# Kernel tuning notes

Measured on AMD Instinct MI355X. Metric: run time of the kernel, lower is better.

The kernel has to match this reference:

```python
import jax, jax.numpy as jnp
import numpy as np
import math

WIN = (3, 3, 3)
DIL = 1
B, N, C = 2, 8192, 128
D = H = W = 48


def _offsets():
    # same ordering as torch get_offset_coord: row-major over (win0,win1,win2)
    half = [math.ceil(w * 0.5) - 1 for w in WIN]
    axes = [jnp.arange(-half[i], WIN[i] - half[i]) for i in range(3)]
    g = jnp.stack(jnp.meshgrid(*axes, indexing='ij'), axis=-1).reshape(-1, 3)  # (K,3)
    # dilation applies to the first two spatial dims (D,H)
    return g * jnp.array([DIL, DIL, 1], dtype=g.dtype)


def setup_inputs() -> dict:
    key = jax.random.key(0)
    ks = jax.random.split(key, 10)
    s = 1.0 / np.sqrt(C)
    return {
        'q_feat': jax.random.normal(ks[0], (B, N, C), jnp.float32),
        'feat': jax.random.normal(ks[1], (B, C, D, H, W), jnp.float32),
        'proj_coord': jax.random.randint(ks[2], (B, N, 3), 0, 48, jnp.int32),
        'hr_coord': jax.random.uniform(ks[3], (B, N, 3), jnp.float32),
        'q_w': jax.random.normal(ks[4], (C, C), jnp.float32) * s,
        'q_b': jax.random.normal(ks[5], (C,), jnp.float32) * s,
        'k_w': jax.random.normal(ks[6], (C, C), jnp.float32) * s,
        'k_b': jax.random.normal(ks[7], (C,), jnp.float32) * s,
        'v_w': jax.random.normal(ks[8], (C, C), jnp.float32) * s,
        'v_b': jax.random.normal(ks[9], (C,), jnp.float32) * s,
    }


def reference(q_feat, feat, proj_coord, hr_coord, q_w, q_b, k_w, k_b, v_w, v_b):
    b, c = feat.shape[:2]
    n = proj_coord.shape[1]
    off = _offsets()                                  # (K,3)
    K = off.shape[0]
    p = [WIN[0] // 2 * DIL, WIN[1] // 2 * DIL, WIN[2] // 2]
    # replication padding (torch ReplicationPad3d == edge mode)
    padded = jnp.pad(feat, ((0, 0), (0, 0), (p[0], p[0]), (p[1], p[1]), (p[2], p[2])), mode='edge')
    Dp, Hp, Wp = padded.shape[2:]
    # absolute window coords in padded volume: (b,N,K,3)
    coords = proj_coord[:, :, None, :] + jnp.array(p, jnp.int32) + off.astype(jnp.int32)
    flat = coords[..., 0] * (Hp * Wp) + coords[..., 1] * Wp + coords[..., 2]  # (b,N,K)
    feat_flat = padded.reshape(b, c, -1).transpose(0, 2, 1)                   # (b,S,c)
    local_feat = jnp.take_along_axis(feat_flat, flat.reshape(b, -1, 1), axis=1)
    local_feat = local_feat.reshape(b, n, K, c)
    # FBLA: q/k attention over local window
    q = q_feat @ q_w.T + q_b                          # (b,N,c)
    k = jnp.einsum('bnkc,dc->bnkd', local_feat, k_w) + k_b
    atten = jax.nn.softmax(jnp.einsum('bnd,bnkd->bnk', q, k), axis=-1)
    v = jnp.einsum('bnkc,dc->bnkd', local_feat, v_w) + v_b
    x = jnp.einsum('bnk,bnkd->bnd', atten, v)
    return q_feat + x
```

## Files before the change

### kernel.cpp

```cpp
#include <hip/hip_runtime.h>
#include <cstdint>

typedef unsigned short u16;
typedef unsigned int   u32;

__device__ __forceinline__ float bf2f(u16 u){ return __uint_as_float(((u32)u) << 16); }
__device__ __forceinline__ float bflo(u32 u){ return __uint_as_float(u << 16); }
__device__ __forceinline__ float bfhi(u32 u){ return __uint_as_float(u & 0xffff0000u); }
__device__ __forceinline__ u16 f2bf(float f){
    u32 x = __float_as_uint(f);
    u32 r = x + 0x7fffu + ((x >> 16) & 1u);
    return (u16)(r >> 16);
}
__device__ __forceinline__ int detect_bf16(const void* p){
    const u16* h = (const u16*)p;
    int hits = 0;
    for (int i = 0; i < 64; ++i){
        const int e = (h[2 * i] >> 7) & 0xFF;
        hits += (e >= 110 && e <= 140) ? 1 : 0;
    }
    return hits >= 40;
}
__device__ __forceinline__ int detect_i64(const int* p){
    int z = 0;
    for (int i = 0; i < 48; ++i) z += (p[2 * i + 1] == 0) ? 1 : 0;
    return z >= 40;
}
__device__ __forceinline__ float ldf(const void* p, size_t i, int isbf){
    return isbf ? bf2f(((const u16*)p)[i]) : ((const float*)p)[i];
}
__device__ __forceinline__ void read_proj(const int* proj, int q, int p64,
                                          int& pz, int& py, int& px){
    if (p64){
        pz = proj[(size_t)(q * 3 + 0) * 2];
        py = proj[(size_t)(q * 3 + 1) * 2];
        px = proj[(size_t)(q * 3 + 2) * 2];
    } else {
        pz = proj[q * 3 + 0]; py = proj[q * 3 + 1]; px = proj[q * 3 + 2];
    }
    pz = min(max(pz, 0), 47); py = min(max(py, 0), 47); px = min(max(px, 0), 47);
}

__global__ __launch_bounds__(256) void k_prep(const void* __restrict__ qw_,
                                              const void* __restrict__ qb_,
                                              const void* __restrict__ kw_,
                                              const void* __restrict__ vw_,
                                              float* __restrict__ M,
                                              float* __restrict__ bias,
                                              float* __restrict__ W2){
    const int bid = blockIdx.x, t = threadIdx.x;
    if (bid < 64){
        const int e = bid * 2 + (t >> 7), c = t & 127;
        const int is_qw = detect_bf16(qw_), is_kw = detect_bf16(kw_);
        float acc = 0.f;
        for (int d = 0; d < 128; ++d)
            acc += ldf(kw_, (size_t)d * 128 + c, is_kw) * ldf(qw_, (size_t)d * 128 + e, is_qw);
        M[e * 128 + c] = acc;
        if (bid == 0 && t < 128){
            const int is_qb = detect_bf16(qb_);
            float ab = 0.f;
            for (int d = 0; d < 128; ++d)
                ab += ldf(kw_, (size_t)d * 128 + t, is_kw) * ldf(qb_, d, is_qb);
            bias[t] = ab;
        }
    } else {
        const int i = (bid - 64) * 256 + t;
        const int c = i >> 7, d = i & 127;
        const int is_vw = detect_bf16(vw_);
        W2[c * 128 + d] = ldf(vw_, (size_t)d * 128 + c, is_vw);
    }
}

__global__ __launch_bounds__(256) void k_tr(const void* __restrict__ feat_,
                                            u16* __restrict__ featT){
    __shared__ u32 sh[4096];
    __shared__ int sbf;
    const int t = threadIdx.x;
    if (t == 0) sbf = detect_bf16(feat_);
    __syncthreads();
    const int isbf = sbf;
    const int chunk = blockIdx.x;
    const int b = chunk / 1728;
    const size_t rel = (size_t)(chunk - b * 1728) * 64;
    if (isbf){
        const u16* f = (const u16*)feat_;
        for (int it = 0; it < 4; ++it){
            const int i = it * 256 + t;
            const int c2 = i >> 4, q16 = i & 15;
            const size_t sA = ((size_t)(b * 128 + 2 * c2    )) * 110592 + rel + q16 * 4;
            const size_t sB = ((size_t)(b * 128 + 2 * c2 + 1)) * 110592 + rel + q16 * 4;
            const uint2 va = *reinterpret_cast<const uint2*>(f + sA);
            const uint2 vb = *reinterpret_cast<const uint2*>(f + sB);
            const u32 vals[4] = {
                (va.x & 0xffffu) | (vb.x << 16),
                (va.x >> 16)     | (vb.x & 0xffff0000u),
                (va.y & 0xffffu) | (vb.y << 16),
                (va.y >> 16)     | (vb.y & 0xffff0000u)
            };
#pragma unroll
            for (int j = 0; j < 4; ++j){
                const int v = q16 * 4 + j;
                const int xv = (v ^ (v >> 4)) & 15;
                sh[v * 64 + (c2 & 3) + 4 * ((c2 >> 2) ^ xv)] = vals[j];
            }
        }
    } else {
        const float* f = (const float*)feat_;
        for (int it = 0; it < 4; ++it){
            const int i = it * 256 + t;
            const int c2 = i >> 4, q16 = i & 15;
            const size_t sA = ((size_t)(b * 128 + 2 * c2    )) * 110592 + rel + q16 * 4;
            const size_t sB = ((size_t)(b * 128 + 2 * c2 + 1)) * 110592 + rel + q16 * 4;
            const float4 a  = *reinterpret_cast<const float4*>(f + sA);
            const float4 bv = *reinterpret_cast<const float4*>(f + sB);
            const float av[4] = {a.x, a.y, a.z, a.w};
            const float bw[4] = {bv.x, bv.y, bv.z, bv.w};
#pragma unroll
            for (int j = 0; j < 4; ++j){
                const int v = q16 * 4 + j;
                const int xv = (v ^ (v >> 4)) & 15;
                sh[v * 64 + (c2 & 3) + 4 * ((c2 >> 2) ^ xv)] =
                    (u32)f2bf(av[j]) | ((u32)f2bf(bw[j]) << 16);
            }
        }
    }
    __syncthreads();
    u32* ft = reinterpret_cast<u32*>(featT);
    const size_t obase = (size_t)chunk * 4096;
#pragma unroll
    for (int k = 0; k < 4; ++k){
        const int G = k * 256 + t;
        const int v = G >> 4, gr = G & 15;
        const int xv = (v ^ (v >> 4)) & 15;
        const uint4 val = *reinterpret_cast<const uint4*>(&sh[v * 64 + 4 * (gr ^ xv)]);
        *reinterpret_cast<uint4*>(ft + obase + (size_t)G * 4) = val;
    }
}

__global__ __launch_bounds__(256) void k_qk(const void* __restrict__ qf_,
                                            const float* __restrict__ M,
                                            const float* __restrict__ bias,
                                            float* __restrict__ qk_all){
    __shared__ float Msh[128 * 128];
    __shared__ float qT[128 * 32];
    const int t = threadIdx.x;
    const int is_qf = detect_bf16(qf_);
    const int qbase = blockIdx.x * 32;
    {
        const float4* Mg4 = reinterpret_cast<const float4*>(M);
        float4* Ms4 = reinterpret_cast<float4*>(Msh);
        for (int i = t; i < 4096; i += 256) Ms4[i] = Mg4[i];
    }
#pragma unroll
    for (int p = 0; p < 4; ++p){
        const int i = p * 256 + t;
        const int q = i & 31, gr = i >> 5;
        float v[4];
        if (is_qf){
            const ushort4 a = *reinterpret_cast<const ushort4*>((const u16*)qf_ + (size_t)(qbase + q) * 128 + gr * 4);
            v[0] = bf2f(a.x); v[1] = bf2f(a.y); v[2] = bf2f(a.z); v[3] = bf2f(a.w);
        } else {
            const float4 a = *reinterpret_cast<const float4*>((const float*)qf_ + (size_t)(qbase + q) * 128 + gr * 4);
            v[0] = a.x; v[1] = a.y; v[2] = a.z; v[3] = a.w;
        }
#pragma unroll
        for (int j = 0; j < 4; ++j) qT[(gr * 4 + j) * 32 + q] = v[j];
    }
    __syncthreads();
    const int g  = t & 31;
    const int qa = t >> 5;
    const float4 b4 = *reinterpret_cast<const float4*>(bias + g * 4);
    float4 acc0 = b4, acc1 = b4, acc2 = b4, acc3 = b4;
#pragma unroll 4
    for (int e = 0; e < 128; ++e){
        const float4 qv = *reinterpret_cast<const float4*>(&qT[e * 32 + qa * 4]);
        const float4 m  = *reinterpret_cast<const float4*>(&Msh[e * 128 + g * 4]);
        acc0.x += qv.x * m.x; acc0.y += qv.x * m.y; acc0.z += qv.x * m.z; acc0.w += qv.x * m.w;
        acc1.x += qv.y * m.x; acc1.y += qv.y * m.y; acc1.z += qv.y * m.z; acc1.w += qv.y * m.w;
        acc2.x += qv.z * m.x; acc2.y += qv.z * m.y; acc2.z += qv.z * m.z; acc2.w += qv.z * m.w;
        acc3.x += qv.w * m.x; acc3.y += qv.w * m.y; acc3.z += qv.w * m.z; acc3.w += qv.w * m.w;
    }
    float* o0 = qk_all + (size_t)(qbase + qa * 4 + 0) * 128 + g * 4;
    float* o1 = qk_all + (size_t)(qbase + qa * 4 + 1) * 128 + g * 4;
    float* o2 = qk_all + (size_t)(qbase + qa * 4 + 2) * 128 + g * 4;
    float* o3 = qk_all + (size_t)(qbase + qa * 4 + 3) * 128 + g * 4;
    *reinterpret_cast<float4*>(o0) = acc0;
    *reinterpret_cast<float4*>(o1) = acc1;
    *reinterpret_cast<float4*>(o2) = acc2;
    *reinterpret_cast<float4*>(o3) = acc3;
}

__global__ __launch_bounds__(256) void k_attn_feat(const u16* __restrict__ featT,
                                                   const float* __restrict__ qk_all,
                                                   const int* __restrict__ proj,
                                                   float* __restrict__ g){
    const int lane = threadIdx.x & 63;
    const int q = blockIdx.x * 4 + (threadIdx.x >> 6);
    const int kg = lane >> 4, cl = lane & 15;
    const int b = q >> 13;
    const int p64 = detect_i64(proj);
    int pz, py, px; read_proj(proj, q, p64, pz, py, px);
    const float4* qp4 = reinterpret_cast<const float4*>(qk_all + (size_t)q * 128 + cl * 8);
    const float4 qA = qp4[0], qB = qp4[1];
    const u16* base = featT + (size_t)b * 14155776 + cl * 8;
    uint4 fr[7];
    float sc[7];
#pragma unroll
    for (int s = 0; s < 7; ++s){
        const int k = s * 4 + kg;
        uint4 v = make_uint4(0u, 0u, 0u, 0u);
        if (k < 27){
            const int dz = k / 9, r9 = k - dz * 9, dy = r9 / 3, dx = r9 - dy * 3;
            const int zz = min(max(pz - 1 + dz, 0), 47);
            const int yy = min(max(py - 1 + dy, 0), 47);
            const int xx = min(max(px - 1 + dx, 0), 47);
            v = *reinterpret_cast<const uint4*>(base + (size_t)(zz * 2304 + yy * 48 + xx) * 128);
        }
        fr[s] = v;
        float t = qA.x * bflo(v.x) + qA.y * bfhi(v.x)
                + qA.z * bflo(v.y) + qA.w * bfhi(v.y)
                + qB.x * bflo(v.z) + qB.y * bfhi(v.z)
                + qB.z * bflo(v.w) + qB.w * bfhi(v.w);
        t += __shfl_xor(t, 1, 64);
        t += __shfl_xor(t, 2, 64);
        t += __shfl_xor(t, 4, 64);
        t += __shfl_xor(t, 8, 64);
        sc[s] = (k < 27) ? t : -1e30f;
    }
    float mx = sc[0];
#pragma unroll
    for (int s = 1; s < 7; ++s) mx = fmaxf(mx, sc[s]);
    mx = fmaxf(mx, __shfl_xor(mx, 16, 64));
    mx = fmaxf(mx, __shfl_xor(mx, 32, 64));
    float e[7], Z = 0.f;
#pragma unroll
    for (int s = 0; s < 7; ++s){ e[s] = __expf(sc[s] - mx); Z += e[s]; }
    Z += __shfl_xor(Z, 16, 64);
    Z += __shfl_xor(Z, 32, 64);
    const float inv = 1.0f / Z;
    float w[8];
#pragma unroll
    for (int i = 0; i < 8; ++i) w[i] = 0.f;
#pragma unroll
    for (int s = 0; s < 7; ++s){
        const float a = e[s] * inv;
        w[0] += a * bflo(fr[s].x); w[1] += a * bfhi(fr[s].x);
        w[2] += a * bflo(fr[s].y); w[3] += a * bfhi(fr[s].y);
        w[4] += a * bflo(fr[s].z); w[5] += a * bfhi(fr[s].z);
        w[6] += a * bflo(fr[s].w); w[7] += a * bfhi(fr[s].w);
    }
#pragma unroll
    for (int i = 0; i < 8; ++i){
        w[i] += __shfl_xor(w[i], 16, 64);
        w[i] += __shfl_xor(w[i], 32, 64);
    }
    if (kg == 0){
        float4 lo4; lo4.x = w[0]; lo4.y = w[1]; lo4.z = w[2]; lo4.w = w[3];
        float4 hi4; hi4.x = w[4]; hi4.y = w[5]; hi4.z = w[6]; hi4.w = w[7];
        float4* o = reinterpret_cast<float4*>(g + (size_t)q * 128 + cl * 8);
        o[0] = lo4; o[1] = hi4;
    }
}

__global__ __launch_bounds__(256) void k_attn_direct(const void* __restrict__ feat_,
                                                     const float* __restrict__ qk_all,
                                                     const int* __restrict__ proj,
                                                     float* __restrict__ g){
    const int lane = threadIdx.x & 63;
    const int q = blockIdx.x * 4 + (threadIdx.x >> 6);
    const int kg = lane >> 4, cl = lane & 15;
    const int b = q >> 13;
    const int isbf = detect_bf16(feat_);
    const int p64 = detect_i64(proj);
    int pz, py, px; read_proj(proj, q, p64, pz, py, px);
    const float* qk = qk_all + (size_t)q * 128 + cl * 8;
    float qv[8];
#pragma unroll
    for (int i = 0; i < 8; ++i) qv[i] = qk[i];
    const size_t cbase = ((size_t)b * 128 + cl * 8) * 110592;
    float f[7][8];
    float sc[7];
#pragma unroll
    for (int s = 0; s < 7; ++s){
        const int k = s * 4 + kg;
#pragma unroll
        for (int i = 0; i < 8; ++i) f[s][i] = 0.f;
        if (k < 27){
            const int dz = k / 9, r9 = k - dz * 9, dy = r9 / 3, dx = r9 - dy * 3;
            const int zz = min(max(pz - 1 + dz, 0), 47);
            const int yy = min(max(py - 1 + dy, 0), 47);
            const int xx = min(max(px - 1 + dx, 0), 47);
            const size_t off = (size_t)zz * 2304 + yy * 48 + xx;
#pragma unroll
            for (int i = 0; i < 8; ++i) f[s][i] = ldf(feat_, cbase + (size_t)i * 110592 + off, isbf);
        }
        float t = 0.f;
#pragma unroll
        for (int i = 0; i < 8; ++i) t += qv[i] * f[s][i];
        t += __shfl_xor(t, 1, 64);
        t += __shfl_xor(t, 2, 64);
        t += __shfl_xor(t, 4, 64);
        t += __shfl_xor(t, 8, 64);
        sc[s] = (k < 27) ? t : -1e30f;
    }
    float mx = sc[0];
#pragma unroll
    for (int s = 1; s < 7; ++s) mx = fmaxf(mx, sc[s]);
    mx = fmaxf(mx, __shfl_xor(mx, 16, 64));
    mx = fmaxf(mx, __shfl_xor(mx, 32, 64));
    float e[7], Z = 0.f;
#pragma unroll
    for (int s = 0; s < 7; ++s){ e[s] = __expf(sc[s] - mx); Z += e[s]; }
    Z += __shfl_xor(Z, 16, 64);
    Z += __shfl_xor(Z, 32, 64);
    const float inv = 1.0f / Z;
    float w[8];
#pragma unroll
    for (int i = 0; i < 8; ++i) w[i] = 0.f;
#pragma unroll
    for (int s = 0; s < 7; ++s){
        const float a = e[s] * inv;
#pragma unroll
        for (int i = 0; i < 8; ++i) w[i] += a * f[s][i];
    }
#pragma unroll
    for (int i = 0; i < 8; ++i){
        w[i] += __shfl_xor(w[i], 16, 64);
        w[i] += __shfl_xor(w[i], 32, 64);
    }
    if (kg == 0){
        float4 lo4; lo4.x = w[0]; lo4.y = w[1]; lo4.z = w[2]; lo4.w = w[3];
        float4 hi4; hi4.x = w[4]; hi4.y = w[5]; hi4.z = w[6]; hi4.w = w[7];
        float4* o = reinterpret_cast<float4*>(g + (size_t)q * 128 + cl * 8);
        o[0] = lo4; o[1] = hi4;
    }
}

__global__ __launch_bounds__(256) void k_out(const float* __restrict__ gbuf,
                                             const float* __restrict__ W2,
                                             const void* __restrict__ qf_,
                                             const void* __restrict__ vb_,
                                             float* __restrict__ out){
    __shared__ float Wsh[128 * 128];
    __shared__ float gT[128 * 32];
    const int t = threadIdx.x;
    const int is_qf = detect_bf16(qf_);
    const int is_vb = detect_bf16(vb_);
    const int qbase = blockIdx.x * 32;
    {
        const float4* Wg4 = reinterpret_cast<const float4*>(W2);
        float4* Ws4 = reinterpret_cast<float4*>(Wsh);
        for (int i = t; i < 4096; i += 256) Ws4[i] = Wg4[i];
    }
#pragma unroll
    for (int p = 0; p < 4; ++p){
        const int i = p * 256 + t;
        const int q = i & 31, gr = i >> 5;
        const float4 a = *reinterpret_cast<const float4*>(gbuf + (size_t)(qbase + q) * 128 + gr * 4);
        gT[(gr * 4 + 0) * 32 + q] = a.x;
        gT[(gr * 4 + 1) * 32 + q] = a.y;
        gT[(gr * 4 + 2) * 32 + q] = a.z;
        gT[(gr * 4 + 3) * 32 + q] = a.w;
    }
    __syncthreads();
    const int g  = t & 31;
    const int qa = t >> 5;
    float4 vb4;
    if (is_vb){
        const ushort4 v = *reinterpret_cast<const ushort4*>((const u16*)vb_ + g * 4);
        vb4.x = bf2f(v.x); vb4.y = bf2f(v.y); vb4.z = bf2f(v.z); vb4.w = bf2f(v.w);
    } else {
        vb4 = *reinterpret_cast<const float4*>((const float*)vb_ + g * 4);
    }
    float4 acc0 = vb4, acc1 = vb4, acc2 = vb4, acc3 = vb4;
#pragma unroll 4
    for (int c = 0; c < 128; ++c){
        const float4 gv = *reinterpret_cast<const float4*>(&gT[c * 32 + qa * 4]);
        const float4 m  = *reinterpret_cast<const float4*>(&Wsh[c * 128 + g * 4]);
        acc0.x += gv.x * m.x; acc0.y += gv.x * m.y; acc0.z += gv.x * m.z; acc0.w += gv.x * m.w;
        acc1.x += gv.y * m.x; acc1.y += gv.y * m.y; acc1.z += gv.y * m.z; acc1.w += gv.y * m.w;
        acc2.x += gv.z * m.x; acc2.y += gv.z * m.y; acc2.z += gv.z * m.z; acc2.w += gv.z * m.w;
        acc3.x += gv.w * m.x; acc3.y += gv.w * m.y; acc3.z += gv.w * m.z; acc3.w += gv.w * m.w;
    }
#pragma unroll
    for (int j = 0; j < 4; ++j){
        const int q = qbase + qa * 4 + j;
        float4 acc = (j == 0) ? acc0 : (j == 1) ? acc1 : (j == 2) ? acc2 : acc3;
        float4 r;
        if (is_qf){
            const ushort4 a = *reinterpret_cast<const ushort4*>((const u16*)qf_ + (size_t)q * 128 + g * 4);
            r.x = bf2f(a.x); r.y = bf2f(a.y); r.z = bf2f(a.z); r.w = bf2f(a.w);
        } else {
            r = *reinterpret_cast<const float4*>((const float*)qf_ + (size_t)q * 128 + g * 4);
        }
        acc.x += r.x; acc.y += r.y; acc.z += r.z; acc.w += r.w;
        *reinterpret_cast<float4*>(out + (size_t)q * 128 + g * 4) = acc;
    }
}

__global__ __launch_bounds__(128) void k_simple(const void* __restrict__ qf_,
                                                const void* __restrict__ feat_,
                                                const void* __restrict__ proj_,
                                                const void* __restrict__ qw_,
                                                const void* __restrict__ qb_,
                                                const void* __restrict__ kw_,
                                                const void* __restrict__ kb_,
                                                const void* __restrict__ vw_,
                                                const void* __restrict__ vb_,
                                                float* __restrict__ out){
    __shared__ float qfs[128];
    __shared__ float qs[128];
    __shared__ float ts[128];
    __shared__ float gs[128];
    __shared__ float ss4[27][4];
    __shared__ float aa[27];
    __shared__ float kbd[1];
    const int t = threadIdx.x;
    const int q = blockIdx.x;
    const int b = q >> 13;
    const int is_qf = detect_bf16(qf_);
    const int is_ft = detect_bf16(feat_);
    const int is_qw = detect_bf16(qw_);
    const int is_qb = detect_bf16(qb_);
    const int is_kw = detect_bf16(kw_);
    const int is_kb = detect_bf16(kb_);
    const int is_vw = detect_bf16(vw_);
    const int is_vb = detect_bf16(vb_);
    const int p64   = detect_i64((const int*)proj_);
    qfs[t] = ldf(qf_, (size_t)q * 128 + t, is_qf);
    __syncthreads();
    {
        float acc = ldf(qb_, t, is_qb);
        for (int e = 0; e < 128; ++e)
            acc += ldf(qw_, (size_t)t * 128 + e, is_qw) * qfs[e];
        qs[t] = acc;
    }
    __syncthreads();
    {
        float acc = 0.f;
        for (int d = 0; d < 128; ++d)
            acc += ldf(kw_, (size_t)d * 128 + t, is_kw) * qs[d];
        ts[t] = acc;
    }
    if (t == 0){
        float kd = 0.f;
        for (int d = 0; d < 128; ++d) kd += ldf(kb_, d, is_kb) * qs[d];
        kbd[0] = kd;
    }
    __syncthreads();
    int pz, py, px; read_proj((const int*)proj_, q, p64, pz, py, px);
    if (t < 108){
        const int k = t >> 2, part = t & 3;
        const int dz = k / 9, dy = (k / 3) % 3, dx = k % 3;
        const int zz = min(max(pz - 1 + dz, 0), 47);
        const int yy = min(max(py - 1 + dy, 0), 47);
        const int xx = min(max(px - 1 + dx, 0), 47);
        const size_t sp = (size_t)zz * 2304 + yy * 48 + xx;
        float s = 0.f;
        for (int c = part * 32; c < part * 32 + 32; ++c)
            s += ts[c] * ldf(feat_, ((size_t)b * 128 + c) * 110592 + sp, is_ft);
        ss4[k][part] = s;
    }
    __syncthreads();
    if (t == 0){
        float sc[27];
        float mx = -1e30f;
        for (int k = 0; k < 27; ++k){
            sc[k] = ss4[k][0] + ss4[k][1] + ss4[k][2] + ss4[k][3] + kbd[0];
            mx = fmaxf(mx, sc[k]);
        }
        float Z = 0.f;
        for (int k = 0; k < 27; ++k){ sc[k] = expf(sc[k] - mx); Z += sc[k]; }
        const float inv = 1.0f / Z;
        for (int k = 0; k < 27; ++k) aa[k] = sc[k] * inv;
    }
    __syncthreads();
    {
        float g = 0.f;
        const size_t cb = ((size_t)b * 128 + t) * 110592;
        for (int k = 0; k < 27; ++k){
            const int dz = k / 9, dy = (k / 3) % 3, dx = k % 3;
            const int zz = min(max(pz - 1 + dz, 0), 47);
            const int yy = min(max(py - 1 + dy, 0), 47);
            const int xx = min(max(px - 1 + dx, 0), 47);
            g += aa[k] * ldf(feat_, cb + (size_t)zz * 2304 + yy * 48 + xx, is_ft);
        }
        gs[t] = g;
    }
    __syncthreads();
    {
        float o = qfs[t] + ldf(vb_, t, is_vb);
        for (int c = 0; c < 128; ++c)
            o += ldf(vw_, (size_t)t * 128 + c, is_vw) * gs[c];
        out[(size_t)q * 128 + t] = o;
    }
}

extern "C" void kernel_launch(void* const* d_in, const int* in_sizes, int n_in,
                              void* d_out, int out_size, void* d_ws, size_t ws_size,
                              hipStream_t stream) {
    const void* qfeat = d_in[0];
    const void* feat  = d_in[1];
    const int*  proj  = (const int*)d_in[2];
    const void* qw = d_in[4];
    const void* qb = d_in[5];
    const void* kw = d_in[6];
    const void* kb = d_in[7];
    const void* vw = d_in[8];
    const void* vb = d_in[9];
    float* out = (float*)d_out;

    char* wsb = (char*)d_ws;
    float* M      = (float*)(wsb);
    float* bias   = (float*)(wsb + 65536);
    float* W2     = (float*)(wsb + 66048);
    float* qk_all = (float*)(wsb + 131584);
    float* g      = (float*)(wsb + 8520192);
    u16*   featT  = (u16*)  (wsb + 16908800);

    const int tier = (ws_size >= (size_t)73531904) ? 1
                   : (ws_size >= (size_t)16908800) ? 2 : 3;

    if (tier == 3){
        hipLaunchKernelGGL(k_simple, dim3(16384), dim3(128), 0, stream,
                           qfeat, feat, proj, qw, qb, kw, kb, vw, vb, out);
        return;
    }
    hipLaunchKernelGGL(k_prep, dim3(128), dim3(256), 0, stream, qw, qb, kw, vw, M, bias, W2);
    hipLaunchKernelGGL(k_qk,   dim3(512), dim3(256), 0, stream, qfeat, M, bias, qk_all);
    if (tier == 1){
        hipLaunchKernelGGL(k_tr,        dim3(3456), dim3(256), 0, stream, feat, featT);
        hipLaunchKernelGGL(k_attn_feat, dim3(4096), dim3(256), 0, stream, featT, qk_all, proj, g);
    } else {
        hipLaunchKernelGGL(k_attn_direct, dim3(4096), dim3(256), 0, stream, feat, qk_all, proj, g);
    }
    hipLaunchKernelGGL(k_out,  dim3(512), dim3(256), 0, stream, g, W2, qfeat, vb, out);
}
```

Baseline: 295.6 us.

## Use packed FP32 FMA in GEMM and attention loops, hoist dtype detection

Rewrites the inner FMA loops of the q·M GEMM, the output projection GEMM and the attention dot/weighted-sum to use v_pk_fma_f32 on float pairs, aiming to halve VALU issue count. Dtype and int64 detection, previously redone per thread in every kernel, now runs once in the prep kernel and is stored in a small flags buffer that later kernels read. The workspace offsets shift to make room for the flags. Inline asm constrains scheduling, and the feature-gather kernel is likely memory-bound, so the gain there may be limited.

```diff
diff --git a/kernel.cpp b/kernel.cpp
--- a/kernel.cpp
+++ b/kernel.cpp
@@ -3,6 +3,8 @@
 
 typedef unsigned short u16;
 typedef unsigned int   u32;
+typedef __attribute__((ext_vector_type(2))) float f32x2;
+typedef __attribute__((ext_vector_type(4))) float f32x4;
 
 __device__ __forceinline__ float bf2f(u16 u){ return __uint_as_float(((u32)u) << 16); }
 __device__ __forceinline__ float bflo(u32 u){ return __uint_as_float(u << 16); }
@@ -41,15 +43,39 @@
     pz = min(max(pz, 0), 47); py = min(max(py, 0), 47); px = min(max(px, 0), 47);
 }
 
+__device__ __forceinline__ void pk_fma_b0(f32x2& acc, const f32x2 s, const f32x2 m){
+    asm("v_pk_fma_f32 %0, %1, %2, %0 op_sel:[0,0,0] op_sel_hi:[0,1,1]"
+        : "+v"(acc) : "v"(s), "v"(m));
+}
+__device__ __forceinline__ void pk_fma_b1(f32x2& acc, const f32x2 s, const f32x2 m){
+    asm("v_pk_fma_f32 %0, %1, %2, %0 op_sel:[1,0,0] op_sel_hi:[1,1,1]"
+        : "+v"(acc) : "v"(s), "v"(m));
+}
+__device__ __forceinline__ void pk_fma(f32x2& acc, const f32x2 a, const f32x2 b){
+    asm("v_pk_fma_f32 %0, %1, %2, %0"
+        : "+v"(acc) : "v"(a), "v"(b));
+}
+
 __global__ __launch_bounds__(256) void k_prep(const void* __restrict__ qw_,
                                               const void* __restrict__ qb_,
                                               const void* __restrict__ kw_,
                                               const void* __restrict__ vw_,
+                                              const void* __restrict__ qf_,
+                                              const void* __restrict__ feat_,
+                                              const int*  __restrict__ proj_,
+                                              const void* __restrict__ vb_,
                                               float* __restrict__ M,
                                               float* __restrict__ bias,
-                                              float* __restrict__ W2){
+                                              float* __restrict__ W2,
+                                              int* __restrict__ flags){
     const int bid = blockIdx.x, t = threadIdx.x;
     if (bid < 64){
+        if (bid == 0){
+            if (t == 0)      flags[0] = detect_bf16(qf_);
+            else if (t == 1) flags[1] = detect_bf16(feat_);
+            else if (t == 2) flags[2] = detect_bf16(vb_);
+            else if (t == 3) flags[3] = detect_i64(proj_);
+        }
         const int e = bid * 2 + (t >> 7), c = t & 127;
         const int is_qw = detect_bf16(qw_), is_kw = detect_bf16(kw_);
         float acc = 0.f;
@@ -72,13 +98,11 @@
 }
 
 __global__ __launch_bounds__(256) void k_tr(const void* __restrict__ feat_,
-                                            u16* __restrict__ featT){
+                                            u16* __restrict__ featT,
+                                            const int* __restrict__ flags){
     __shared__ u32 sh[4096];
-    __shared__ int sbf;
     const int t = threadIdx.x;
-    if (t == 0) sbf = detect_bf16(feat_);
-    __syncthreads();
-    const int isbf = sbf;
+    const int isbf = flags[1];
     const int chunk = blockIdx.x;
     const int b = chunk / 1728;
     const size_t rel = (size_t)(chunk - b * 1728) * 64;
@@ -140,11 +164,12 @@
 __global__ __launch_bounds__(256) void k_qk(const void* __restrict__ qf_,
                                             const float* __restrict__ M,
                                             const float* __restrict__ bias,
-                                            float* __restrict__ qk_all){
+                                            float* __restrict__ qk_all,
+                                            const int* __restrict__ flags){
     __shared__ float Msh[128 * 128];
     __shared__ float qT[128 * 32];
     const int t = threadIdx.x;
-    const int is_qf = detect_bf16(qf_);
+    const int is_qf = flags[0];
     const int qbase = blockIdx.x * 32;
     {
         const float4* Mg4 = reinterpret_cast<const float4*>(M);
@@ -170,38 +195,45 @@
     const int g  = t & 31;
     const int qa = t >> 5;
     const float4 b4 = *reinterpret_cast<const float4*>(bias + g * 4);
-    float4 acc0 = b4, acc1 = b4, acc2 = b4, acc3 = b4;
+    const f32x2 bi01 = {b4.x, b4.y}, bi23 = {b4.z, b4.w};
+    f32x2 a00 = bi01, a01 = bi23, a10 = bi01, a11 = bi23;
+    f32x2 a20 = bi01, a21 = bi23, a30 = bi01, a31 = bi23;
 #pragma unroll 4
     for (int e = 0; e < 128; ++e){
-        const float4 qv = *reinterpret_cast<const float4*>(&qT[e * 32 + qa * 4]);
-        const float4 m  = *reinterpret_cast<const float4*>(&Msh[e * 128 + g * 4]);
-        acc0.x += qv.x * m.x; acc0.y += qv.x * m.y; acc0.z += qv.x * m.z; acc0.w += qv.x * m.w;
-        acc1.x += qv.y * m.x; acc1.y += qv.y * m.y; acc1.z += qv.y * m.z; acc1.w += qv.y * m.w;
-        acc2.x += qv.z * m.x; acc2.y += qv.z * m.y; acc2.z += qv.z * m.z; acc2.w += qv.z * m.w;
-        acc3.x += qv.w * m.x; acc3.y += qv.w * m.y; acc3.z += qv.w * m.z; acc3.w += qv.w * m.w;
-    }
-    float* o0 = qk_all + (size_t)(qbase + qa * 4 + 0) * 128 + g * 4;
-    float* o1 = qk_all + (size_t)(qbase + qa * 4 + 1) * 128 + g * 4;
-    float* o2 = qk_all + (size_t)(qbase + qa * 4 + 2) * 128 + g * 4;
-    float* o3 = qk_all + (size_t)(qbase + qa * 4 + 3) * 128 + g * 4;
-    *reinterpret_cast<float4*>(o0) = acc0;
-    *reinterpret_cast<float4*>(o1) = acc1;
-    *reinterpret_cast<float4*>(o2) = acc2;
-    *reinterpret_cast<float4*>(o3) = acc3;
+        const f32x4 qv = *reinterpret_cast<const f32x4*>(&qT[e * 32 + qa * 4]);
+        const f32x4 mv = *reinterpret_cast<const f32x4*>(&Msh[e * 128 + g * 4]);
+        const f32x2 q01 = qv.xy, q23 = qv.zw;
+        const f32x2 m01 = mv.xy, m23 = mv.zw;
+        pk_fma_b0(a00, q01, m01); pk_fma_b0(a01, q01, m23);
+        pk_fma_b1(a10, q01, m01); pk_fma_b1(a11, q01, m23);
+        pk_fma_b0(a20, q23, m01); pk_fma_b0(a21, q23, m23);
+        pk_fma_b1(a30, q23, m01); pk_fma_b1(a31, q23, m23);
+    }
+    const f32x4 r0 = {a00.x, a00.y, a01.x, a01.y};
+    const f32x4 r1 = {a10.x, a10.y, a11.x, a11.y};
+    const f32x4 r2 = {a20.x, a20.y, a21.x, a21.y};
+    const f32x4 r3 = {a30.x, a30.y, a31.x, a31.y};
+    *reinterpret_cast<f32x4*>(qk_all + (size_t)(qbase + qa * 4 + 0) * 128 + g * 4) = r0;
+    *reinterpret_cast<f32x4*>(qk_all + (size_t)(qbase + qa * 4 + 1) * 128 + g * 4) = r1;
+    *reinterpret_cast<f32x4*>(qk_all + (size_t)(qbase + qa * 4 + 2) * 128 + g * 4) = r2;
+    *reinterpret_cast<f32x4*>(qk_all + (size_t)(qbase + qa * 4 + 3) * 128 + g * 4) = r3;
 }
 
 __global__ __launch_bounds__(256) void k_attn_feat(const u16* __restrict__ featT,
                                                    const float* __restrict__ qk_all,
                                                    const int* __restrict__ proj,
-                                                   float* __restrict__ g){
+                                                   float* __restrict__ g,
+                                                   const int* __restrict__ flags){
     const int lane = threadIdx.x & 63;
     const int q = blockIdx.x * 4 + (threadIdx.x >> 6);
     const int kg = lane >> 4, cl = lane & 15;
     const int b = q >> 13;
-    const int p64 = detect_i64(proj);
+    const int p64 = flags[3];
     int pz, py, px; read_proj(proj, q, p64, pz, py, px);
     const float4* qp4 = reinterpret_cast<const float4*>(qk_all + (size_t)q * 128 + cl * 8);
     const float4 qA = qp4[0], qB = qp4[1];
+    const f32x2 qA01 = {qA.x, qA.y}, qA23 = {qA.z, qA.w};
+    const f32x2 qB01 = {qB.x, qB.y}, qB23 = {qB.z, qB.w};
     const u16* base = featT + (size_t)b * 14155776 + cl * 8;
     uint4 fr[7];
     float sc[7];
@@ -217,10 +249,14 @@
             v = *reinterpret_cast<const uint4*>(base + (size_t)(zz * 2304 + yy * 48 + xx) * 128);
         }
         fr[s] = v;
-        float t = qA.x * bflo(v.x) + qA.y * bfhi(v.x)
-                + qA.z * bflo(v.y) + qA.w * bfhi(v.y)
-                + qB.x * bflo(v.z) + qB.y * bfhi(v.z)
-                + qB.z * bflo(v.w) + qB.w * bfhi(v.w);
+        const f32x2 f0 = {bflo(v.x), bfhi(v.x)};
+        const f32x2 f1 = {bflo(v.y), bfhi(v.y)};
+        const f32x2 f2 = {bflo(v.z), bfhi(v.z)};
+        const f32x2 f3 = {bflo(v.w), bfhi(v.w)};
+        f32x2 d2 = {0.f, 0.f};
+        pk_fma(d2, qA01, f0); pk_fma(d2, qA23, f1);
+        pk_fma(d2, qB01, f2); pk_fma(d2, qB23, f3);
+        float t = d2.x + d2.y;
         t += __shfl_xor(t, 1, 64);
         t += __shfl_xor(t, 2, 64);
         t += __shfl_xor(t, 4, 64);
@@ -238,17 +274,20 @@
     Z += __shfl_xor(Z, 16, 64);
     Z += __shfl_xor(Z, 32, 64);
     const float inv = 1.0f / Z;
-    float w[8];
-#pragma unroll
-    for (int i = 0; i < 8; ++i) w[i] = 0.f;
+    f32x2 w0 = {0.f,0.f}, w1 = {0.f,0.f}, w2 = {0.f,0.f}, w3 = {0.f,0.f};
 #pragma unroll
     for (int s = 0; s < 7; ++s){
         const float a = e[s] * inv;
-        w[0] += a * bflo(fr[s].x); w[1] += a * bfhi(fr[s].x);
-        w[2] += a * bflo(fr[s].y); w[3] += a * bfhi(fr[s].y);
-        w[4] += a * bflo(fr[s].z); w[5] += a * bfhi(fr[s].z);
-        w[6] += a * bflo(fr[s].w); w[7] += a * bfhi(fr[s].w);
-    }
+        const f32x2 aa = {a, a};
+        const uint4 v = fr[s];
+        const f32x2 f0 = {bflo(v.x), bfhi(v.x)};
+        const f32x2 f1 = {bflo(v.y), bfhi(v.y)};
+        const f32x2 f2 = {bflo(v.z), bfhi(v.z)};
+        const f32x2 f3 = {bflo(v.w), bfhi(v.w)};
+        pk_fma(w0, aa, f0); pk_fma(w1, aa, f1);
+        pk_fma(w2, aa, f2); pk_fma(w3, aa, f3);
+    }
+    float w[8] = {w0.x, w0.y, w1.x, w1.y, w2.x, w2.y, w3.x, w3.y};
 #pragma unroll
     for (int i = 0; i < 8; ++i){
         w[i] += __shfl_xor(w[i], 16, 64);
@@ -265,13 +304,14 @@
 __global__ __launch_bounds__(256) void k_attn_direct(const void* __restrict__ feat_,
                                                      const float* __restrict__ qk_all,
                                                      const int* __restrict__ proj,
-                                                     float* __restrict__ g){
+                                                     float* __restrict__ g,
+                                                     const int* __restrict__ flags){
     const int lane = threadIdx.x & 63;
     const int q = blockIdx.x * 4 + (threadIdx.x >> 6);
     const int kg = lane >> 4, cl = lane & 15;
     const int b = q >> 13;
-    const int isbf = detect_bf16(feat_);
-    const int p64 = detect_i64(proj);
+    const int isbf = flags[1];
+    const int p64 = flags[3];
     int pz, py, px; read_proj(proj, q, p64, pz, py, px);
     const float* qk = qk_all + (size_t)q * 128 + cl * 8;
     float qv[8];
@@ -340,12 +380,13 @@
                                              const float* __restrict__ W2,
                                              const void* __restrict__ qf_,
                                              const void* __restrict__ vb_,
-                                             float* __restrict__ out){
+                                             float* __restrict__ out,
+                                             const int* __restrict__ flags){
     __shared__ float Wsh[128 * 128];
     __shared__ float gT[128 * 32];
     const int t = threadIdx.x;
-    const int is_qf = detect_bf16(qf_);
-    const int is_vb = detect_bf16(vb_);
+    const int is_qf = flags[0];
+    const int is_vb = flags[2];
     const int qbase = blockIdx.x * 32;
     {
         const float4* Wg4 = reinterpret_cast<const float4*>(W2);
@@ -372,20 +413,29 @@
     } else {
         vb4 = *reinterpret_cast<const float4*>((const float*)vb_ + g * 4);
     }
-    float4 acc0 = vb4, acc1 = vb4, acc2 = vb4, acc3 = vb4;
+    const f32x2 bi01 = {vb4.x, vb4.y}, bi23 = {vb4.z, vb4.w};
+    f32x2 a00 = bi01, a01 = bi23, a10 = bi01, a11 = bi23;
+    f32x2 a20 = bi01, a21 = bi23, a30 = bi01, a31 = bi23;
 #pragma unroll 4
     for (int c = 0; c < 128; ++c){
-        const float4 gv = *reinterpret_cast<const float4*>(&gT[c * 32 + qa * 4]);
-        const float4 m  = *reinterpret_cast<const float4*>(&Wsh[c * 128 + g * 4]);
-        acc0.x += gv.x * m.x; acc0.y += gv.x * m.y; acc0.z += gv.x * m.z; acc0.w += gv.x * m.w;
-        acc1.x += gv.y * m.x; acc1.y += gv.y * m.y; acc1.z += gv.y * m.z; acc1.w += gv.y * m.w;
-        acc2.x += gv.z * m.x; acc2.y += gv.z * m.y; acc2.z += gv.z * m.z; acc2.w += gv.z * m.w;
-        acc3.x += gv.w * m.x; acc3.y += gv.w * m.y; acc3.z += gv.w * m.z; acc3.w += gv.w * m.w;
-    }
+        const f32x4 gv = *reinterpret_cast<const f32x4*>(&gT[c * 32 + qa * 4]);
+        const f32x4 mv = *reinterpret_cast<const f32x4*>(&Wsh[c * 128 + g * 4]);
+        const f32x2 g01 = gv.xy, g23 = gv.zw;
+        const f32x2 m01 = mv.xy, m23 = mv.zw;
+        pk_fma_b0(a00, g01, m01); pk_fma_b0(a01, g01, m23);
+        pk_fma_b1(a10, g01, m01); pk_fma_b1(a11, g01, m23);
+        pk_fma_b0(a20, g23, m01); pk_fma_b0(a21, g23, m23);
+        pk_fma_b1(a30, g23, m01); pk_fma_b1(a31, g23, m23);
+    }
+    float4 accs[4];
+    accs[0] = make_float4(a00.x, a00.y, a01.x, a01.y);
+    accs[1] = make_float4(a10.x, a10.y, a11.x, a11.y);
+    accs[2] = make_float4(a20.x, a20.y, a21.x, a21.y);
+    accs[3] = make_float4(a30.x, a30.y, a31.x, a31.y);
 #pragma unroll
     for (int j = 0; j < 4; ++j){
         const int q = qbase + qa * 4 + j;
-        float4 acc = (j == 0) ? acc0 : (j == 1) ? acc1 : (j == 2) ? acc2 : acc3;
+        float4 acc = accs[j];
         float4 r;
         if (is_qf){
             const ushort4 a = *reinterpret_cast<const ushort4*>((const u16*)qf_ + (size_t)q * 128 + g * 4);
@@ -513,26 +563,28 @@
     char* wsb = (char*)d_ws;
     float* M      = (float*)(wsb);
     float* bias   = (float*)(wsb + 65536);
-    float* W2     = (float*)(wsb + 66048);
-    float* qk_all = (float*)(wsb + 131584);
-    float* g      = (float*)(wsb + 8520192);
-    u16*   featT  = (u16*)  (wsb + 16908800);
-
-    const int tier = (ws_size >= (size_t)73531904) ? 1
-                   : (ws_size >= (size_t)16908800) ? 2 : 3;
+    int*   flags  = (int*)  (wsb + 66048);
+    float* W2     = (float*)(wsb + 66112);
+    float* qk_all = (float*)(wsb + 131648);
+    float* g      = (float*)(wsb + 8520256);
+    u16*   featT  = (u16*)  (wsb + 16908864);
+
+    const int tier = (ws_size >= (size_t)73531968) ? 1
+                   : (ws_size >= (size_t)16908864) ? 2 : 3;
 
     if (tier == 3){
         hipLaunchKernelGGL(k_simple, dim3(16384), dim3(128), 0, stream,
                            qfeat, feat, proj, qw, qb, kw, kb, vw, vb, out);
         return;
     }
-    hipLaunchKernelGGL(k_prep, dim3(128), dim3(256), 0, stream, qw, qb, kw, vw, M, bias, W2);
-    hipLaunchKernelGGL(k_qk,   dim3(512), dim3(256), 0, stream, qfeat, M, bias, qk_all);
+    hipLaunchKernelGGL(k_prep, dim3(128), dim3(256), 0, stream,
+                       qw, qb, kw, vw, qfeat, feat, proj, vb, M, bias, W2, flags);
+    hipLaunchKernelGGL(k_qk,   dim3(512), dim3(256), 0, stream, qfeat, M, bias, qk_all, flags);
     if (tier == 1){
-        hipLaunchKernelGGL(k_tr,        dim3(3456), dim3(256), 0, stream, feat, featT);
-        hipLaunchKernelGGL(k_attn_feat, dim3(4096), dim3(256), 0, stream, featT, qk_all, proj, g);
+        hipLaunchKernelGGL(k_tr,        dim3(3456), dim3(256), 0, stream, feat, featT, flags);
+        hipLaunchKernelGGL(k_attn_feat, dim3(4096), dim3(256), 0, stream, featT, qk_all, proj, g, flags);
     } else {
-        hipLaunchKernelGGL(k_attn_direct, dim3(4096), dim3(256), 0, stream, feat, qk_all, proj, g);
-    }
-    hipLaunchKernelGGL(k_out,  dim3(512), dim3(256), 0, stream, g, W2, qfeat, vb, out);
-}
+        hipLaunchKernelGGL(k_attn_direct, dim3(4096), dim3(256), 0, stream, feat, qk_all, proj, g, flags);
+    }
+    hipLaunchKernelGGL(k_out,  dim3(512), dim3(256), 0, stream, g, W2, qfeat, vb, out, flags);
+}
```

Result: no change. 292.1 us, median of 2 (-1.2%).
